# Kernel tuning notes

Measured on AMD Instinct MI355X. Metric: run time of the kernel, lower is better.

The kernel has to match this reference:

```python
import jax, jax.numpy as jnp
import numpy as np

N = 40960          # total nodes in batch of session graphs
S = 4096           # number of sessions (segments)
E = 81920          # directed edges
D = 64             # embedding_dim
H = 100            # hidden_dim
F_IN = 5 * D + 1   # 321, price + 5 concatenated embeddings
V_ITEMS = 50000
NUM_ITER = 1


def setup_inputs() -> dict:
    key = jax.random.key(0)
    ks = jax.random.split(key, 30)
    rn = lambda k, shape, s=0.05: (jax.random.normal(k, shape, jnp.float32) * s)
    ri = lambda k, shape, hi: jax.random.randint(k, shape, 0, hi, jnp.int64)
    return {
        "price": rn(ks[0], (N, 1), 1.0),
        "category": ri(ks[1], (N,), 256),
        "sub_category": ri(ks[2], (N,), 1024),
        "element": ri(ks[3], (N,), 2048),
        "brand": ri(ks[4], (N,), 4096),
        "product_id": ri(ks[5], (N,), V_ITEMS),
        "edge_index": ri(ks[6], (2, E), N),
        "batch": jnp.repeat(jnp.arange(S, dtype=jnp.int64), N // S),  # sorted segment ids, 10 nodes/session
        "emb_cat": rn(ks[7], (256, D)),
        "emb_sub": rn(ks[8], (1024, D)),
        "emb_elem": rn(ks[9], (2048, D)),
        "emb_brand": rn(ks[10], (4096, D)),
        "emb_item": rn(ks[11], (V_ITEMS, D)),
        "W_msg": rn(ks[12], (F_IN, H)),
        "b_msg": rn(ks[13], (H,)),
        "W_ih": rn(ks[14], (H, 3 * H)),
        "W_hh": rn(ks[15], (H, 3 * H)),
        "b_ih": rn(ks[16], (3 * H,)),
        "b_hh": rn(ks[17], (3 * H,)),
        "W_last": rn(ks[18], (F_IN, H)),
        "b_last": rn(ks[19], (H,)),
        "W_g1": rn(ks[20], (H, H)),
        "b_g1": rn(ks[21], (H,)),
        "W_g2": rn(ks[22], (H, 1)),
        "b_g2": rn(ks[23], (1,)),
        "W_fc": rn(ks[24], (H, V_ITEMS)),
        "b_fc": rn(ks[25], (V_ITEMS,)),
    }


def _gru_cell(x, h, W_ih, W_hh, b_ih, b_hh):
    # torch.nn.GRUCell math, gates ordered [r, z, n]
    gi = x @ W_ih + b_ih                     # [N, 3H]
    gh = h @ W_hh + b_hh                     # [N, 3H]
    i_r, i_z, i_n = jnp.split(gi, 3, axis=1)
    h_r, h_z, h_n = jnp.split(gh, 3, axis=1)
    r = jax.nn.sigmoid(i_r + h_r)
    z = jax.nn.sigmoid(i_z + h_z)
    n = jnp.tanh(i_n + r * h_n)
    return (1.0 - z) * n + z * h


def reference(price, category, sub_category, element, brand, product_id,
              edge_index, batch,
              emb_cat, emb_sub, emb_elem, emb_brand, emb_item,
              W_msg, b_msg, W_ih, W_hh, b_ih, b_hh,
              W_last, b_last, W_g1, b_g1, W_g2, b_g2, W_fc, b_fc):
    # ----- NodeEmbedding: 5 gathers + price concat -> [N, 321] -----
    x = jnp.concatenate([
        price,
        emb_cat[category], emb_sub[sub_category], emb_elem[element],
        emb_brand[brand], emb_item[product_id],
    ], axis=1)

    # ----- GRUGraphLayer: message_linear, then mean-aggregate + GRUCell -----
    h = x @ W_msg + b_msg                                     # [N, H]
    src, dst = edge_index[0], edge_index[1]
    deg = jax.ops.segment_sum(jnp.ones((E,), jnp.float32), dst, num_segments=N)
    inv_deg = jnp.where(deg > 0, 1.0 / jnp.maximum(deg, 1.0), 0.0)[:, None]
    for _ in range(NUM_ITER):
        msg = jax.ops.segment_sum(h[src], dst, num_segments=N) * inv_deg  # mean aggr
        h = _gru_cell(msg, h, W_ih, W_hh, b_ih, b_hh)

    # ----- last-visited node per session (scatter_max on arange -> last index) -----
    last_idx = jax.ops.segment_max(jnp.arange(N, dtype=jnp.int64), batch, num_segments=S)
    last = x[last_idx] @ W_last + b_last                       # [S, H]
    h = h + last[batch]                                        # broadcast back to nodes

    # ----- AttentionalAggregation: gate MLP + segment softmax + weighted sum -----
    # (dropout is inference no-op)
    gate = (jax.nn.relu(h @ W_g1 + b_g1) @ W_g2 + b_g2)[:, 0]  # [N]
    gmax = jax.ops.segment_max(gate, batch, num_segments=S)
    w = jnp.exp(gate - gmax[batch])
    wsum = jax.ops.segment_sum(w, batch, num_segments=S)
    alpha = w / wsum[batch]                                    # [N]
    pooled = jax.ops.segment_sum(alpha[:, None] * h, batch, num_segments=S)  # [S, H]

    # ----- final scoring over item catalog -----
    return pooled @ W_fc + b_fc                                # [S, V_ITEMS]
```

## Files before the change

### kernel.cpp

```cpp
#include <hip/hip_runtime.h>
#include <hip/hip_bf16.h>

#define N_NODES 40960
#define N_SESS  4096
#define N_EDGES 81920
#define DIM     64
#define HID     100
#define VITEMS  50000

__global__ __launch_bounds__(256)
void gemm_f32(const float* __restrict__ A, int lda,
              const float* __restrict__ B, int ldb,
              const float* __restrict__ bias,
              float* __restrict__ C, int ldc,
              int M, int N, int K, int relu)
{
    __shared__ float As[32][68];
    __shared__ float Bs[32][68];
    const int tid = threadIdx.x;
    const int tm = tid & 15;
    const int tn = tid >> 4;
    const int m0 = blockIdx.y * 64;
    const int n0 = blockIdx.x * 64;
    float acc[4][4] = {};

    for (int k0 = 0; k0 < K; k0 += 32) {
        #pragma unroll
        for (int i = 0; i < 2; ++i) {
            int f4  = tid + i * 256;
            int row = f4 >> 3;
            int kc  = (f4 & 7) << 2;
            float4 v = make_float4(0.f, 0.f, 0.f, 0.f);
            int gm = m0 + row, gk = k0 + kc;
            if (gm < M && gk < K)
                v = *reinterpret_cast<const float4*>(&A[(size_t)gm * lda + gk]);
            As[kc + 0][row] = v.x;
            As[kc + 1][row] = v.y;
            As[kc + 2][row] = v.z;
            As[kc + 3][row] = v.w;
        }
        #pragma unroll
        for (int i = 0; i < 2; ++i) {
            int f4  = tid + i * 256;
            int row = f4 >> 4;
            int nc  = (f4 & 15) << 2;
            float4 v = make_float4(0.f, 0.f, 0.f, 0.f);
            int gk = k0 + row, gn = n0 + nc;
            if (gk < K && gn < N)
                v = *reinterpret_cast<const float4*>(&B[(size_t)gk * ldb + gn]);
            *reinterpret_cast<float4*>(&Bs[row][nc]) = v;
        }
        __syncthreads();
        #pragma unroll
        for (int kk = 0; kk < 32; ++kk) {
            float4 a4 = *reinterpret_cast<const float4*>(&As[kk][tm << 2]);
            float4 b4 = *reinterpret_cast<const float4*>(&Bs[kk][tn << 2]);
            float av[4] = {a4.x, a4.y, a4.z, a4.w};
            float bv[4] = {b4.x, b4.y, b4.z, b4.w};
            #pragma unroll
            for (int i = 0; i < 4; ++i)
                #pragma unroll
                for (int j = 0; j < 4; ++j)
                    acc[i][j] += av[i] * bv[j];
        }
        __syncthreads();
    }

    const int gn0 = n0 + (tn << 2);
    if (gn0 >= N) return;
    float4 bi = make_float4(0.f, 0.f, 0.f, 0.f);
    if (bias) bi = *reinterpret_cast<const float4*>(&bias[gn0]);
    #pragma unroll
    for (int i = 0; i < 4; ++i) {
        int gm = m0 + (tm << 2) + i;
        if (gm >= M) continue;
        float4 o = make_float4(acc[i][0] + bi.x, acc[i][1] + bi.y,
                               acc[i][2] + bi.z, acc[i][3] + bi.w);
        if (relu) {
            o.x = fmaxf(o.x, 0.f); o.y = fmaxf(o.y, 0.f);
            o.z = fmaxf(o.z, 0.f); o.w = fmaxf(o.w, 0.f);
        }
        *reinterpret_cast<float4*>(&C[(size_t)gm * ldc + gn0]) = o;
    }
}

__global__ void h0_gather(const float* __restrict__ price,
                          const int* __restrict__ cat, const int* __restrict__ sub,
                          const int* __restrict__ elem, const int* __restrict__ brand,
                          const int* __restrict__ pid,
                          const float* __restrict__ Wmsg, const float* __restrict__ b_msg,
                          const float* __restrict__ Pm, float* __restrict__ h0)
{
    int idx = blockIdx.x * 256 + threadIdx.x;
    if (idx >= N_NODES * HID) return;
    int n = idx / HID, j = idx - n * HID;
    float v = b_msg[j] + price[n] * Wmsg[j];
    v += Pm[(size_t)(        cat[n]) * HID + j];
    v += Pm[(size_t)( 256 +  sub[n]) * HID + j];
    v += Pm[(size_t)(1280 + elem[n]) * HID + j];
    v += Pm[(size_t)(3328 + brand[n]) * HID + j];
    v += Pm[(size_t)(7424 +  pid[n]) * HID + j];
    h0[idx] = v;
}

__global__ void deg_count(const int* __restrict__ dst, float* __restrict__ deg)
{
    int e = blockIdx.x * 256 + threadIdx.x;
    if (e < N_EDGES) atomicAdd(&deg[dst[e]], 1.0f);
}

__global__ void inv_deg_k(float* __restrict__ deg)
{
    int n = blockIdx.x * 256 + threadIdx.x;
    if (n < N_NODES) {
        float d = deg[n];
        deg[n] = d > 0.f ? 1.0f / d : 0.0f;
    }
}

__global__ void msg_scatter(const int* __restrict__ src, const int* __restrict__ dst,
                            const float* __restrict__ h0, float* __restrict__ msg)
{
    int idx = blockIdx.x * 256 + threadIdx.x;
    if (idx >= N_EDGES * HID) return;
    int e = idx / HID, j = idx - e * HID;
    atomicAdd(&msg[(size_t)dst[e] * HID + j], h0[(size_t)src[e] * HID + j]);
}

__global__ void msg_scale(const float* __restrict__ inv_deg, float* __restrict__ msg)
{
    int idx = blockIdx.x * 256 + threadIdx.x;
    if (idx >= N_NODES * HID) return;
    int n = idx / HID;
    msg[idx] *= inv_deg[n];
}

__global__ void gru_gates(const float* __restrict__ gi, const float* __restrict__ gh,
                          float* __restrict__ h)
{
    int idx = blockIdx.x * 256 + threadIdx.x;
    if (idx >= 10240 * HID) return;
    int nl = idx / HID, j = idx - nl * HID;
    float ir  = gi[nl * 300 + j],        hr = gh[nl * 300 + j];
    float iz  = gi[nl * 300 + 100 + j],  hz = gh[nl * 300 + 100 + j];
    float in_ = gi[nl * 300 + 200 + j],  hn = gh[nl * 300 + 200 + j];
    float r  = 1.f / (1.f + expf(-(ir + hr)));
    float z  = 1.f / (1.f + expf(-(iz + hz)));
    float nn = tanhf(in_ + r * hn);
    float hv = h[idx];
    h[idx] = (1.f - z) * nn + z * hv;
}

__global__ void last_idx_k(const int* __restrict__ batch, int* __restrict__ last_idx)
{
    int n = blockIdx.x * 256 + threadIdx.x;
    if (n < N_NODES) atomicMax(&last_idx[batch[n]], n);
}

__global__ __launch_bounds__(256)
void last_proj(const int* __restrict__ last_idx, const float* __restrict__ price,
               const int* __restrict__ cat, const int* __restrict__ sub,
               const int* __restrict__ elem, const int* __restrict__ brand,
               const int* __restrict__ pid,
               const float* __restrict__ Ecat, const float* __restrict__ Esub,
               const float* __restrict__ Eelem, const float* __restrict__ Ebrand,
               const float* __restrict__ Eitem,
               const float* __restrict__ W_last, const float* __restrict__ b_last,
               float* __restrict__ last)
{
    int s = blockIdx.x * 4 + (threadIdx.x >> 6);
    int l = threadIdx.x & 63;
    int n = last_idx[s];
    int ci = cat[n] * DIM, si = sub[n] * DIM, ei = elem[n] * DIM;
    int bi = brand[n] * DIM, pi = pid[n] * DIM;
    float acc0 = 0.f, acc1 = 0.f;
    for (int k = 0; k < 321; ++k) {
        float xk;
        if (k == 0)       xk = price[n];
        else if (k < 65)  xk = Ecat[ci + k - 1];
        else if (k < 129) xk = Esub[si + k - 65];
        else if (k < 193) xk = Eelem[ei + k - 129];
        else if (k < 257) xk = Ebrand[bi + k - 193];
        else              xk = Eitem[pi + k - 257];
        acc0 += xk * W_last[k * HID + l];
        if (l < HID - 64) acc1 += xk * W_last[k * HID + 64 + l];
    }
    last[s * HID + l] = acc0 + b_last[l];
    if (l < HID - 64) last[s * HID + 64 + l] = acc1 + b_last[64 + l];
}

__global__ void add_last(const int* __restrict__ batch, const float* __restrict__ last,
                         float* __restrict__ h)
{
    int idx = blockIdx.x * 256 + threadIdx.x;
    if (idx >= N_NODES * HID) return;
    int n = idx / HID, j = idx - n * HID;
    h[idx] += last[(size_t)batch[n] * HID + j];
}

__global__ __launch_bounds__(256)
void gate_reduce(const float* __restrict__ g1, const float* __restrict__ W_g2,
                 const float* __restrict__ b_g2, const int* __restrict__ batch,
                 float* __restrict__ gate, unsigned* __restrict__ gmax)
{
    int n = blockIdx.x * 4 + (threadIdx.x >> 6);
    int l = threadIdx.x & 63;
    float s = g1[(size_t)n * HID + l] * W_g2[l];
    if (l < HID - 64) s += g1[(size_t)n * HID + 64 + l] * W_g2[64 + l];
    #pragma unroll
    for (int off = 32; off > 0; off >>= 1) s += __shfl_xor(s, off, 64);
    if (l == 0) {
        float gt = s + b_g2[0];
        gate[n] = gt;
        unsigned u = __float_as_uint(gt);
        u = (u & 0x80000000u) ? ~u : (u | 0x80000000u);
        atomicMax(&gmax[batch[n]], u);
    }
}

__global__ void softmax_w(const int* __restrict__ batch, const unsigned* __restrict__ gmax,
                          float* __restrict__ gate, float* __restrict__ wsum)
{
    int n = blockIdx.x * 256 + threadIdx.x;
    if (n >= N_NODES) return;
    unsigned u = gmax[batch[n]];
    float gm = (u & 0x80000000u) ? __uint_as_float(u ^ 0x80000000u) : __uint_as_float(~u);
    float w = expf(gate[n] - gm);
    gate[n] = w;
    atomicAdd(&wsum[batch[n]], w);
}

__global__ void pooled_k(const int* __restrict__ batch, const float* __restrict__ gate,
                         const float* __restrict__ wsum, const float* __restrict__ h,
                         float* __restrict__ pooled)
{
    int idx = blockIdx.x * 256 + threadIdx.x;
    if (idx >= N_NODES * HID) return;
    int n = idx / HID, j = idx - n * HID;
    int b = batch[n];
    float alpha = gate[n] / wsum[b];
    atomicAdd(&pooled[(size_t)b * HID + j], alpha * h[idx]);
}

extern "C" void kernel_launch(void* const* d_in, const int* in_sizes, int n_in,
                              void* d_out, int out_size, void* d_ws, size_t ws_size,
                              hipStream_t stream)
{
    const float* price    = (const float*)d_in[0];
    const int*   cat      = (const int*)d_in[1];
    const int*   sub      = (const int*)d_in[2];
    const int*   elem     = (const int*)d_in[3];
    const int*   brand    = (const int*)d_in[4];
    const int*   pid      = (const int*)d_in[5];
    const int*   eidx     = (const int*)d_in[6];
    const int*   batch    = (const int*)d_in[7];
    const float* emb_cat  = (const float*)d_in[8];
    const float* emb_sub  = (const float*)d_in[9];
    const float* emb_elem = (const float*)d_in[10];
    const float* emb_brand= (const float*)d_in[11];
    const float* emb_item = (const float*)d_in[12];
    const float* W_msg    = (const float*)d_in[13];
    const float* b_msg    = (const float*)d_in[14];
    const float* W_ih     = (const float*)d_in[15];
    const float* W_hh     = (const float*)d_in[16];
    const float* b_ih     = (const float*)d_in[17];
    const float* b_hh     = (const float*)d_in[18];
    const float* W_last   = (const float*)d_in[19];
    const float* b_last   = (const float*)d_in[20];
    const float* W_g1     = (const float*)d_in[21];
    const float* b_g1     = (const float*)d_in[22];
    const float* W_g2     = (const float*)d_in[23];
    const float* b_g2     = (const float*)d_in[24];
    const float* W_fc     = (const float*)d_in[25];
    const float* b_fc     = (const float*)d_in[26];
    float* out = (float*)d_out;

    const int* src = eidx;
    const int* dst = eidx + N_EDGES;

    float* w = (float*)d_ws;
    float*    msg    = w + 0;
    float*    deg    = w + 4096000;
    float*    wsum   = w + 4136960;
    float*    pooled = w + 4141056;
    int*      lastix = (int*)(w + 4550656);
    unsigned* gmax   = (unsigned*)(w + 4554752);
    float*    Pm     = w + 4558848;
    float*    h0     = w + 10301248;
    float*    gi     = w + 14397248;
    float*    gh     = w + 17469248;
    float*    last   = w + 20541248;
    float*    gate   = w + 20950848;

    hipMemsetAsync(w, 0, (size_t)4558848 * sizeof(float), stream);

    dim3 blk(256);
    auto gemm = [&](const float* A, int lda, const float* B, int ldb,
                    const float* bias, float* C, int ldc, int M, int N, int K, int relu) {
        dim3 g((N + 63) / 64, (M + 63) / 64);
        hipLaunchKernelGGL(gemm_f32, g, blk, 0, stream, A, lda, B, ldb, bias, C, ldc, M, N, K, relu);
    };

    gemm(emb_cat,   DIM, W_msg +   1 * HID, HID, nullptr, Pm +      0, HID,   256, HID, DIM, 0);
    gemm(emb_sub,   DIM, W_msg +  65 * HID, HID, nullptr, Pm +  25600, HID,  1024, HID, DIM, 0);
    gemm(emb_elem,  DIM, W_msg + 129 * HID, HID, nullptr, Pm + 128000, HID,  2048, HID, DIM, 0);
    gemm(emb_brand, DIM, W_msg + 193 * HID, HID, nullptr, Pm + 332800, HID,  4096, HID, DIM, 0);
    gemm(emb_item,  DIM, W_msg + 257 * HID, HID, nullptr, Pm + 742400, HID, VITEMS, HID, DIM, 0);

    h0_gather<<<16000, blk, 0, stream>>>(price, cat, sub, elem, brand, pid, W_msg, b_msg, Pm, h0);

    deg_count<<<320, blk, 0, stream>>>(dst, deg);
    inv_deg_k<<<160, blk, 0, stream>>>(deg);
    msg_scatter<<<32000, blk, 0, stream>>>(src, dst, h0, msg);
    msg_scale<<<16000, blk, 0, stream>>>(deg, msg);

    for (int c = 0; c < 4; ++c) {
        size_t nb = (size_t)c * 10240;
        gemm(msg + nb * HID, HID, W_ih, 300, b_ih, gi, 300, 10240, 300, HID, 0);
        gemm(h0  + nb * HID, HID, W_hh, 300, b_hh, gh, 300, 10240, 300, HID, 0);
        gru_gates<<<4000, blk, 0, stream>>>(gi, gh, h0 + nb * HID);
    }

    last_idx_k<<<160, blk, 0, stream>>>(batch, lastix);
    last_proj<<<1024, blk, 0, stream>>>(lastix, price, cat, sub, elem, brand, pid,
                                        emb_cat, emb_sub, emb_elem, emb_brand, emb_item,
                                        W_last, b_last, last);
    add_last<<<16000, blk, 0, stream>>>(batch, last, h0);

    gemm(h0, HID, W_g1, HID, b_g1, msg , HID, N_NODES, HID, HID, 1);
    gate_reduce<<<10240, blk, 0, stream>>>(msg, W_g2, b_g2, batch, gate, gmax);
    softmax_w<<<160, blk, 0, stream>>>(batch, gmax, gate, wsum);
    pooled_k<<<16000, blk, 0, stream>>>(batch, gate, wsum, h0, pooled);

    gemm(pooled, HID, W_fc, VITEMS, b_fc, out, VITEMS, N_SESS, VITEMS, HID, 0);
}
```

Baseline: 1.955 ms.

## Run final scoring GEMM on bf16 MFMA with split-precision hi/lo operands

Replaces the fp32 SIMT GEMM for the pooled×W_fc scoring with a matrix-core kernel. Both operands are split into bf16 high and low parts and combined with three MFMA products (hh, lh, hl) to keep near-fp32 accuracy. W_fc is transposed into padded K=128 bf16 buffers by a separate kernel, and pooled is split the same way. Each block keeps its A fragments in registers and sweeps a chunk of N tiles. The cost is extra conversion passes and dropping the lo×lo term, which gives slight precision loss.

```diff
diff --git a/kernel.cpp b/kernel.cpp
--- a/kernel.cpp
+++ b/kernel.cpp
@@ -7,6 +7,17 @@
 #define DIM     64
 #define HID     100
 #define VITEMS  50000
+
+typedef short s16x8 __attribute__((ext_vector_type(8)));
+typedef float f32x4 __attribute__((ext_vector_type(4)));
+
+__device__ __forceinline__ unsigned short f2bf(float f) {
+    unsigned u = __float_as_uint(f);
+    return (unsigned short)((u + 0x7FFFu + ((u >> 16) & 1u)) >> 16);
+}
+__device__ __forceinline__ float bf2f(unsigned short s) {
+    return __uint_as_float(((unsigned)s) << 16);
+}
 
 __global__ __launch_bounds__(256)
 void gemm_f32(const float* __restrict__ A, int lda,
@@ -81,6 +92,103 @@
             o.z = fmaxf(o.z, 0.f); o.w = fmaxf(o.w, 0.f);
         }
         *reinterpret_cast<float4*>(&C[(size_t)gm * ldc + gn0]) = o;
+    }
+}
+
+__global__ __launch_bounds__(256)
+void b_split(const float* __restrict__ Wfc, unsigned short* __restrict__ Bh,
+             unsigned short* __restrict__ Bl)
+{
+    __shared__ unsigned short Hs[64][136];
+    __shared__ unsigned short Ls[64][136];
+    const int n0 = blockIdx.x * 64;
+    const int nn = threadIdx.x & 63, kk = threadIdx.x >> 6;
+    for (int k = kk; k < 128; k += 4) {
+        float v = 0.f;
+        int n = n0 + nn;
+        if (k < HID && n < VITEMS) v = Wfc[(size_t)k * VITEMS + n];
+        unsigned short h = f2bf(v);
+        Hs[nn][k] = h;
+        Ls[nn][k] = f2bf(v - bf2f(h));
+    }
+    __syncthreads();
+    const int row = threadIdx.x >> 2, part = threadIdx.x & 3;
+    size_t base = (size_t)(n0 + row) * 128 + part * 32;
+    #pragma unroll
+    for (int c = 0; c < 4; ++c) {
+        *reinterpret_cast<s16x8*>(&Bh[base + c * 8]) =
+            *reinterpret_cast<const s16x8*>(&Hs[row][part * 32 + c * 8]);
+        *reinterpret_cast<s16x8*>(&Bl[base + c * 8]) =
+            *reinterpret_cast<const s16x8*>(&Ls[row][part * 32 + c * 8]);
+    }
+}
+
+__global__ void a_split(const float* __restrict__ pooled, unsigned short* __restrict__ Ah,
+                        unsigned short* __restrict__ Al)
+{
+    int idx = blockIdx.x * 256 + threadIdx.x;
+    if (idx >= N_SESS * 128) return;
+    int m = idx >> 7, k = idx & 127;
+    float v = (k < HID) ? pooled[m * HID + k] : 0.f;
+    unsigned short h = f2bf(v);
+    Ah[idx] = h;
+    Al[idx] = f2bf(v - bf2f(h));
+}
+
+__global__ __launch_bounds__(256)
+void score_gemm(const unsigned short* __restrict__ Ah, const unsigned short* __restrict__ Al,
+                const unsigned short* __restrict__ Bh, const unsigned short* __restrict__ Bl,
+                const float* __restrict__ bias, float* __restrict__ out)
+{
+    const int chunk = blockIdx.x & 7;
+    const int m0    = (blockIdx.x >> 3) * 64;
+    const int w     = threadIdx.x >> 6;
+    const int l     = threadIdx.x & 63;
+    const int lm    = l & 15;
+    const int lk    = l >> 4;
+
+    s16x8 ah[4][4], al[4][4];
+    #pragma unroll
+    for (int mf = 0; mf < 4; ++mf)
+        #pragma unroll
+        for (int ks = 0; ks < 4; ++ks) {
+            size_t off = (size_t)(m0 + mf * 16 + lm) * 128 + ks * 32 + lk * 8;
+            ah[mf][ks] = *reinterpret_cast<const s16x8*>(Ah + off);
+            al[mf][ks] = *reinterpret_cast<const s16x8*>(Al + off);
+        }
+
+    const int t0 = chunk * 98;
+    const int t1 = (t0 + 98 < 782) ? t0 + 98 : 782;
+    for (int nt = t0; nt < t1; ++nt) {
+        const int n0 = nt * 64 + w * 16;
+        f32x4 acc[4];
+        #pragma unroll
+        for (int mf = 0; mf < 4; ++mf) acc[mf] = (f32x4){0.f, 0.f, 0.f, 0.f};
+
+        #pragma unroll
+        for (int ks = 0; ks < 4; ++ks) {
+            size_t boff = (size_t)(n0 + lm) * 128 + ks * 32 + lk * 8;
+            s16x8 bh = *reinterpret_cast<const s16x8*>(Bh + boff);
+            s16x8 bl = *reinterpret_cast<const s16x8*>(Bl + boff);
+            #pragma unroll
+            for (int mf = 0; mf < 4; ++mf) {
+                acc[mf] = __builtin_amdgcn_mfma_f32_16x16x32_bf16(ah[mf][ks], bh, acc[mf], 0, 0, 0);
+                acc[mf] = __builtin_amdgcn_mfma_f32_16x16x32_bf16(al[mf][ks], bh, acc[mf], 0, 0, 0);
+                acc[mf] = __builtin_amdgcn_mfma_f32_16x16x32_bf16(ah[mf][ks], bl, acc[mf], 0, 0, 0);
+            }
+        }
+
+        const int n = n0 + lm;
+        if (n < VITEMS) {
+            const float bv = bias[n];
+            #pragma unroll
+            for (int mf = 0; mf < 4; ++mf) {
+                const int mbase = m0 + mf * 16 + lk * 4;
+                #pragma unroll
+                for (int r = 0; r < 4; ++r)
+                    out[(size_t)(mbase + r) * VITEMS + n] = acc[mf][r] + bv;
+            }
+        }
     }
 }
 
@@ -292,6 +400,11 @@
     float*    last   = w + 20541248;
     float*    gate   = w + 20950848;
 
+    unsigned short* Bth = (unsigned short*)msg;
+    unsigned short* Btl = (unsigned short*)gi;
+    unsigned short* Ahp = (unsigned short*)Pm;
+    unsigned short* Alp = (unsigned short*)(Pm + 262144);
+
     hipMemsetAsync(w, 0, (size_t)4558848 * sizeof(float), stream);
 
     dim3 blk(256);
@@ -329,8 +442,12 @@
 
     gemm(h0, HID, W_g1, HID, b_g1, msg , HID, N_NODES, HID, HID, 1);
     gate_reduce<<<10240, blk, 0, stream>>>(msg, W_g2, b_g2, batch, gate, gmax);
+
+    b_split<<<782, blk, 0, stream>>>(W_fc, Bth, Btl);
+
     softmax_w<<<160, blk, 0, stream>>>(batch, gmax, gate, wsum);
     pooled_k<<<16000, blk, 0, stream>>>(batch, gate, wsum, h0, pooled);
 
-    gemm(pooled, HID, W_fc, VITEMS, b_fc, out, VITEMS, N_SESS, VITEMS, HID, 0);
-}
+    a_split<<<2048, blk, 0, stream>>>(pooled, Ahp, Alp);
+    score_gemm<<<512, blk, 0, stream>>>(Ahp, Alp, Bth, Btl, b_fc, out);
+}
```

New measurement: 1.778 ms. 1.1x faster.
